# Kernel optimization log

Hardware: AMD Instinct MI355X
Metric: run time of the kernel (lower is better)

The kernel has to match this reference:

```python
import jax, jax.numpy as jnp
import numpy as np

B, C, H, W = 4, 96, 64, 64
N_STATE, DT_RANK, K = 16, 6, 3


def _layernorm(x, g, b, eps=1e-5):
    m = jnp.mean(x, axis=-1, keepdims=True)
    v = jnp.mean((x - m) ** 2, axis=-1, keepdims=True)
    return (x - m) / jnp.sqrt(v + eps) * g + b


def _grid_sample(img, gx, gy):
    # F.grid_sample: bilinear, align_corners=True, zeros padding; gx,gy in [-1,1], [B,Ho,Wo]
    Bc, Cc, Hi, Wi = img.shape
    fx = (gx + 1.0) * 0.5 * (Wi - 1)
    fy = (gy + 1.0) * 0.5 * (Hi - 1)
    x0 = jnp.floor(fx)
    y0 = jnp.floor(fy)
    wx1 = fx - x0
    wy1 = fy - y0

    def tap(ix, iy, w):
        valid = ((ix >= 0) & (ix < Wi) & (iy >= 0) & (iy < Hi)).astype(img.dtype)
        ic = jnp.clip(ix, 0, Wi - 1).astype(jnp.int32)
        jc = jnp.clip(iy, 0, Hi - 1).astype(jnp.int32)
        v = jax.vmap(lambda im, yy, xx: im[:, yy, xx])(img, jc, ic)  # [B,C,Ho,Wo]
        return v * (w * valid)[:, None, :, :]

    return (tap(x0, y0, (1 - wx1) * (1 - wy1)) + tap(x0 + 1, y0, wx1 * (1 - wy1))
            + tap(x0, y0 + 1, (1 - wx1) * wy1) + tap(x0 + 1, y0 + 1, wx1 * wy1))


def _resize_bilinear(img, Ho, Wo):
    # torch F.interpolate(mode='bilinear', align_corners=False)
    Bc, Cc, Hi, Wi = img.shape

    def src(n_out, n_in):
        s = jnp.maximum((jnp.arange(n_out, dtype=img.dtype) + 0.5) * (n_in / n_out) - 0.5, 0.0)
        i0 = jnp.floor(s).astype(jnp.int32)
        i1 = jnp.minimum(i0 + 1, n_in - 1)
        return i0, i1, s - i0

    y0, y1, wy = src(Ho, Hi)
    x0, x1, wx = src(Wo, Wi)
    row = img[:, :, y0, :] * (1 - wy)[None, None, :, None] + img[:, :, y1, :] * wy[None, None, :, None]
    return row[:, :, :, x0] * (1 - wx) + row[:, :, :, x1] * wx


def _conv_offset(x, conv1_w, conv1_b, ca1_w, ca1_b, ca2_w, ca2_b, ln_g, ln_b, conv2_w):
    Bc, Cc = x.shape[:2]
    p = conv1_w.shape[-1] // 2
    x1 = jax.lax.conv_general_dilated(
        x, conv1_w, (1, 1), [(p, p), (p, p)],
        dimension_numbers=("NCHW", "OIHW", "NCHW"), feature_group_count=Cc
    ) + conv1_b[None, :, None, None]
    xc = jnp.mean(x, axis=(2, 3))  # adaptive_avg_pool2d -> (1,1)
    hid = jax.nn.gelu(xc @ ca1_w.T + ca1_b, approximate=False)
    ca = jax.nn.sigmoid(hid @ ca2_w.T + ca2_b)
    x1 = x1 * ca[:, :, None, None]
    xn = _layernorm(jnp.transpose(x1, (0, 2, 3, 1)), ln_g, ln_b)
    xg = jax.nn.gelu(jnp.transpose(xn, (0, 3, 1, 2)), approximate=False)
    return jnp.einsum("bchw,oc->bohw", xg, conv2_w[:, :, 0, 0])


def _deformable(x, rpe_table, conv1_w, conv1_b, ca1_w, ca1_b, ca2_w, ca2_b, ln_g, ln_b, conv2_w):
    Bc, Cc, Hc, Wc = x.shape
    L = Hc * Wc
    off = _conv_offset(x, conv1_w, conv1_b, ca1_w, ca1_b, ca2_w, ca2_b, ln_g, ln_b, conv2_w)
    offset = off[:, :2]
    de = off[:, 2]
    rng = jnp.array([1.0 / (Hc - 1.0), 1.0 / (Wc - 1.0)], off.dtype).reshape(1, 2, 1, 1)
    offset = jnp.transpose(jnp.tanh(offset) * rng, (0, 2, 3, 1))  # [B,H,W,2] (dy,dx)
    ry = (jnp.linspace(0.5, Hc - 0.5, Hc) / (Hc - 1.0)) * 2.0 - 1.0
    rx = (jnp.linspace(0.5, Wc - 0.5, Wc) / (Wc - 1.0)) * 2.0 - 1.0
    ref = jnp.stack(jnp.meshgrid(ry, rx, indexing="ij"), -1)  # [H,W,2] (y,x)
    pos = offset + ref[None]
    de_index = jnp.tanh(de).reshape(Bc, L)
    path_ref = (jnp.linspace(0.5, L - 0.5, L) / (L - 1.0)) * 2.0 - 1.0
    path_pos = de_index + path_ref[None]
    x_sampled = _grid_sample(x, pos[..., 1], pos[..., 0])
    rpe = jnp.broadcast_to(rpe_table[None], (Bc,) + rpe_table.shape)
    rpe_bias = _resize_bilinear(rpe, Hc, Wc)
    ky = (jnp.linspace(0.0, float(Hc), Hc) / (Hc - 1.0)) * 2.0 - 1.0
    kx = (jnp.linspace(0.0, float(Wc), Wc) / (Wc - 1.0)) * 2.0 - 1.0
    key_grid = jnp.stack(jnp.meshgrid(ky, kx, indexing="ij"), -1)
    disp = (key_grid[None] - pos) * 0.5
    pos_bias = _grid_sample(rpe_bias, disp[..., 1], disp[..., 0])
    xd = (x_sampled + pos_bias).reshape(Bc, Cc, L)
    indices = jnp.argsort(path_pos, axis=-1)  # topk(k=N, largest=False) == ascending argsort
    xs2 = jnp.take_along_axis(xd, indices[:, None, :], axis=2)
    return xs2, indices


def _selective_scan(u, delta, A, Bs, Cs, Dv, delta_bias):
    Bc, KD, L = u.shape
    Kk = Bs.shape[1]
    Dd = KD // Kk
    Ns = A.shape[1]
    delta = jax.nn.softplus(delta + delta_bias[None, :, None])
    dt4 = jnp.moveaxis(delta.reshape(Bc, Kk, Dd, L), 3, 0)
    u4 = jnp.moveaxis(u.reshape(Bc, Kk, Dd, L), 3, 0)
    Bt = jnp.moveaxis(Bs, 3, 0)
    Ct = jnp.moveaxis(Cs, 3, 0)
    A3 = A.reshape(Kk, Dd, Ns)

    @jax.checkpoint
    def step(h, inp):
        dt, ut, bt, ct = inp  # [B,K,D],[B,K,D],[B,K,N],[B,K,N]
        h = jnp.exp(dt[..., None] * A3) * h + (dt * ut)[..., None] * bt[:, :, None, :]
        return h, jnp.einsum("bkdn,bkn->bkd", h, ct)

    h0 = jnp.zeros((Bc, Kk, Dd, Ns), u.dtype)
    _, ys = jax.lax.scan(step, h0, (dt4, u4, Bt, Ct))
    ys = jnp.moveaxis(ys, 0, 3).reshape(Bc, KD, L)
    return ys + u * Dv[None, :, None]


def _forward(x, x_proj_weight, dt_projs_weight, dt_projs_bias, A_logs, Ds_param,
             conv1_w, conv1_b, ca1_w, ca1_b, ca2_w, ca2_b, ln_g, ln_b, conv2_w, rpe_table):
    Bc, Dd, Hc, Wc = x.shape
    L = Hc * Wc
    Kk, _, R = dt_projs_weight.shape
    Ns = A_logs.shape[1]
    xs0 = x.reshape(Bc, Dd, L)
    xs2, indices = _deformable(x, rpe_table, conv1_w, conv1_b, ca1_w, ca1_b, ca2_w, ca2_b, ln_g, ln_b, conv2_w)
    xs = jnp.stack([xs0, xs0[..., ::-1], xs2], axis=1)  # [B,3,D,L]
    x_dbl = jnp.einsum("bkdl,kcd->bkcl", xs, x_proj_weight)
    dts, Bs, Cs = jnp.split(x_dbl, [R, R + Ns], axis=2)
    dts = jnp.einsum("bkrl,kdr->bkdl", dts, dt_projs_weight)
    A = -jnp.exp(A_logs)
    ys = _selective_scan(xs.reshape(Bc, Kk * Dd, L), dts.reshape(Bc, Kk * Dd, L),
                         A, Bs, Cs, Ds_param, dt_projs_bias.reshape(-1))
    ys = ys.reshape(Bc, Kk, Dd, L)
    inv = jnp.argsort(indices, axis=-1)  # inverse permutation (DeformableLayerReverse)
    y2 = jnp.take_along_axis(ys[:, 2], inv[:, None, :], axis=2)
    y = (ys[:, 0] + ys[:, 1][..., ::-1] + y2) / 3.0
    return jnp.transpose(y, (0, 2, 1)).reshape(Bc, Hc, Wc, Dd)


def setup_inputs():
    key = jax.random.key(0)
    ks = jax.random.split(key, 12)
    f = jnp.float32
    return {
        "x": jax.random.normal(ks[0], (B, C, H, W), f),
        "x_proj_weight": jax.random.normal(ks[1], (K, DT_RANK + 2 * N_STATE, C), f) * 0.05,
        "dt_projs_weight": jax.random.normal(ks[2], (K, C, DT_RANK), f) * 0.05,
        "dt_projs_bias": jax.random.normal(ks[3], (K, C), f) * 0.1,
        "A_logs": jnp.tile(jnp.log(jnp.arange(1, N_STATE + 1, dtype=f))[None, :], (K * C, 1)),
        "Ds_param": jnp.ones((K * C,), f),
        "conv1_w": jax.random.normal(ks[4], (C, 1, 9, 9), f) * 0.05,
        "conv1_b": jnp.zeros((C,), f),
        "ca1_w": jax.random.normal(ks[5], (C // 16, C), f) * 0.1,
        "ca1_b": jnp.zeros((C // 16,), f),
        "ca2_w": jax.random.normal(ks[6], (C, C // 16), f) * 0.1,
        "ca2_b": jnp.zeros((C,), f),
        "ln_g": jnp.ones((C,), f),
        "ln_b": jnp.zeros((C,), f),
        "conv2_w": jax.random.normal(ks[7], (3, C, 1, 1), f) * 0.05,
        "rpe_table": jax.random.normal(ks[8], (C, 7, 7), f) * 0.01,
    }


def reference(x, x_proj_weight, dt_projs_weight, dt_projs_bias, A_logs, Ds_param,
              conv1_w, conv1_b, ca1_w, ca1_b, ca2_w, ca2_b, ln_g, ln_b, conv2_w, rpe_table):
    return _forward(x, x_proj_weight, dt_projs_weight, dt_projs_bias, A_logs, Ds_param,
                    conv1_w, conv1_b, ca1_w, ca1_b, ca2_w, ca2_b, ln_g, ln_b, conv2_w, rpe_table)
```

## Files before the change

### kernel.cpp

```cpp
#include <hip/hip_runtime.h>

#define BB 4
#define CC 96
#define HH 64
#define WW 64
#define LL 4096
#define KK 3
#define RR 6
#define NN 16

__device__ __forceinline__ float geluf(float x){
    return 0.5f * x * (1.0f + erff(x * 0.70710678118654752f));
}
__device__ __forceinline__ float softplusf(float x){
    return fmaxf(x, 0.0f) + log1pf(expf(-fabsf(x)));
}
__device__ __forceinline__ float sigmoidf(float x){
    return 1.0f / (1.0f + expf(-x));
}

__global__ __launch_bounds__(256) void k_mean(const float* __restrict__ x, float* __restrict__ xc){
    int bc = blockIdx.x;
    const float* p = x + (size_t)bc * LL;
    float s = 0.f;
    for (int i = threadIdx.x; i < LL; i += 256) s += p[i];
    __shared__ float red[256];
    red[threadIdx.x] = s; __syncthreads();
    for (int st = 128; st > 0; st >>= 1){
        if (threadIdx.x < st) red[threadIdx.x] += red[threadIdx.x + st];
        __syncthreads();
    }
    if (threadIdx.x == 0) xc[bc] = red[0] * (1.0f / LL);
}

__global__ __launch_bounds__(128) void k_ca(const float* __restrict__ xc,
                     const float* __restrict__ w1, const float* __restrict__ b1,
                     const float* __restrict__ w2, const float* __restrict__ b2,
                     float* __restrict__ ca){
    int b = blockIdx.x;
    int t = threadIdx.x;
    __shared__ float hid[CC/16];
    if (t < CC/16){
        float a = b1[t];
        for (int d = 0; d < CC; d++) a += w1[t*CC + d] * xc[b*CC + d];
        hid[t] = geluf(a);
    }
    __syncthreads();
    if (t < CC){
        float a = b2[t];
        #pragma unroll
        for (int i = 0; i < CC/16; i++) a += w2[t*(CC/16) + i] * hid[i];
        ca[b*CC + t] = sigmoidf(a);
    }
}

__global__ __launch_bounds__(256) void k_conv(const float* __restrict__ x, const float* __restrict__ w,
                       const float* __restrict__ bias, const float* __restrict__ ca,
                       float* __restrict__ x1){
    int tid4 = blockIdx.x * 256 + threadIdx.x;
    int wq4 = (tid4 & 15) * 4;
    int rest = tid4 >> 4;
    int h = rest & 63;
    int bc = rest >> 6;
    int c = bc % CC; int b = bc / CC;
    const float* xp = x + (size_t)bc * LL;
    const float* wp = w + c * 81;
    float a0 = 0.f, a1 = 0.f, a2 = 0.f, a3 = 0.f;
    #pragma unroll
    for (int ky = 0; ky < 9; ky++){
        int yy = h + ky - 4;
        if (yy < 0 || yy >= HH) continue;
        const float4* row4 = (const float4*)(xp + yy*WW);
        int g = wq4 >> 2;
        float4 q0 = (wq4 >= 4)  ? row4[g-1] : make_float4(0.f,0.f,0.f,0.f);
        float4 q1 = row4[g];
        float4 q2 = (wq4 < 60)  ? row4[g+1] : make_float4(0.f,0.f,0.f,0.f);
        float v[12] = {q0.x,q0.y,q0.z,q0.w, q1.x,q1.y,q1.z,q1.w, q2.x,q2.y,q2.z,q2.w};
        const float* wr = wp + ky*9;
        #pragma unroll
        for (int kx = 0; kx < 9; kx++){
            float wk = wr[kx];
            a0 = fmaf(v[kx],   wk, a0);
            a1 = fmaf(v[kx+1], wk, a1);
            a2 = fmaf(v[kx+2], wk, a2);
            a3 = fmaf(v[kx+3], wk, a3);
        }
    }
    float sc = ca[b*CC + c];
    float bb = bias[c];
    float4 o = make_float4((a0+bb)*sc, (a1+bb)*sc, (a2+bb)*sc, (a3+bb)*sc);
    *(float4*)(x1 + (size_t)bc*LL + h*WW + wq4) = o;
}

__global__ __launch_bounds__(256) void k_rpe(const float* __restrict__ t, float* __restrict__ out){
    int gid = blockIdx.x * 256 + threadIdx.x;
    int l = gid & (LL-1); int c = gid >> 12;
    int h = l >> 6, w = l & 63;
    float sy = fmaxf((h + 0.5f) * (7.0f/64.0f) - 0.5f, 0.f);
    float sx = fmaxf((w + 0.5f) * (7.0f/64.0f) - 0.5f, 0.f);
    int y0 = (int)floorf(sy); int x0 = (int)floorf(sx);
    float wy = sy - (float)y0, wx = sx - (float)x0;
    int y1 = min(y0 + 1, 6), x1i = min(x0 + 1, 6);
    const float* tp = t + c * 49;
    float r0 = tp[y0*7 + x0] * (1.f - wy) + tp[y1*7 + x0] * wy;
    float r1 = tp[y0*7 + x1i] * (1.f - wy) + tp[y1*7 + x1i] * wy;
    out[gid] = r0 * (1.f - wx) + r1 * wx;
}

__global__ __launch_bounds__(256) void k_off(const float* __restrict__ x1,
                      const float* __restrict__ g, const float* __restrict__ bta,
                      const float* __restrict__ w2,
                      float* __restrict__ posy, float* __restrict__ posx, float* __restrict__ path){
    int blk = blockIdx.x;
    int ltile = blk & 63; int b = blk >> 6;
    int lane = threadIdx.x & 63;
    int wg = threadIdx.x >> 6;
    int l = ltile * 64 + lane;
    const float* p = x1 + (size_t)b * CC * LL + l;
    float v[24];
    float s = 0.f, ss = 0.f;
    #pragma unroll
    for (int j = 0; j < 24; j++){
        float t = p[(size_t)(wg*24 + j) * LL];
        v[j] = t; s += t; ss += t*t;
    }
    __shared__ float ls[4][64], lss[4][64];
    ls[wg][lane] = s; lss[wg][lane] = ss;
    __syncthreads();
    s  = ls[0][lane]  + ls[1][lane]  + ls[2][lane]  + ls[3][lane];
    ss = lss[0][lane] + lss[1][lane] + lss[2][lane] + lss[3][lane];
    float m = s * (1.0f/CC);
    float rstd = rsqrtf(ss*(1.0f/CC) - m*m + 1e-5f);
    float a0 = 0.f, a1 = 0.f, a2 = 0.f;
    #pragma unroll
    for (int j = 0; j < 24; j++){
        int c = wg*24 + j;
        float xn = (v[j]-m)*rstd*g[c] + bta[c];
        float xg = geluf(xn);
        a0 = fmaf(w2[c],      xg, a0);
        a1 = fmaf(w2[CC+c],   xg, a1);
        a2 = fmaf(w2[2*CC+c], xg, a2);
    }
    __shared__ float la[3][4][64];
    la[0][wg][lane] = a0; la[1][wg][lane] = a1; la[2][wg][lane] = a2;
    __syncthreads();
    if (wg < 3){
        float a = la[wg][0][lane] + la[wg][1][lane] + la[wg][2][lane] + la[wg][3][lane];
        int h = l >> 6, w = l & 63;
        if (wg == 0)      posy[b*LL + l] = tanhf(a)*(1.0f/63.0f) + ((2*h+1)*(1.0f/63.0f) - 1.0f);
        else if (wg == 1) posx[b*LL + l] = tanhf(a)*(1.0f/63.0f) + ((2*w+1)*(1.0f/63.0f) - 1.0f);
        else              path[b*LL + l] = tanhf(a) + ((l + 0.5f)*(2.0f/4095.0f) - 1.0f);
    }
}

__device__ __forceinline__ float bilin0(const float* __restrict__ img, float gx, float gy){
    float fx = (gx + 1.f) * 31.5f;
    float fy = (gy + 1.f) * 31.5f;
    float x0f = floorf(fx), y0f = floorf(fy);
    float wx = fx - x0f, wy = fy - y0f;
    int x0 = (int)x0f, y0 = (int)y0f;
    float acc = 0.f;
    bool vx0 = (x0 >= 0) & (x0 < WW), vx1 = (x0+1 >= 0) & (x0+1 < WW);
    bool vy0 = (y0 >= 0) & (y0 < HH), vy1 = (y0+1 >= 0) & (y0+1 < HH);
    if (vy0 & vx0) acc += img[y0*WW + x0]       * (1.f-wx) * (1.f-wy);
    if (vy0 & vx1) acc += img[y0*WW + x0+1]     * wx       * (1.f-wy);
    if (vy1 & vx0) acc += img[(y0+1)*WW + x0]   * (1.f-wx) * wy;
    if (vy1 & vx1) acc += img[(y0+1)*WW + x0+1] * wx       * wy;
    return acc;
}

typedef unsigned long long u64s;
__device__ __forceinline__ u64s shflx64(u64s x, int m){
    int lo = __shfl_xor((int)(unsigned)x, m);
    int hi = __shfl_xor((int)(unsigned)(x >> 32), m);
    return ((u64s)(unsigned)hi << 32) | (unsigned)lo;
}
__device__ __forceinline__ void cex(u64s& a, u64s& b, bool up){
    u64s mn = a < b ? a : b;
    u64s mx = a < b ? b : a;
    a = up ? mn : mx;
    b = up ? mx : mn;
}
__global__ __launch_bounds__(1024) void k_sortsample(
        const float* __restrict__ path, int* __restrict__ idx, int* __restrict__ inv,
        const float* __restrict__ x, const float* __restrict__ rpe,
        const float* __restrict__ posy, const float* __restrict__ posx,
        float* __restrict__ xd){
    int blk = blockIdx.x;
    if (blk < BB){
        int b = blk;
        int t = threadIdx.x;
        __shared__ u64s lds[LL];
        u64s v[4];
        #pragma unroll
        for (int r = 0; r < 4; r++){
            int e = t*4 + r;
            unsigned u = __float_as_uint(path[b*LL + e]);
            u ^= (u >> 31) ? 0xFFFFFFFFu : 0x80000000u;
            v[r] = ((u64s)u << 32) | (unsigned)e;
        }
        for (int kk = 2; kk <= LL; kk <<= 1){
            for (int j = kk >> 1; j > 0; j >>= 1){
                if (j >= 256){
                    __syncthreads();
                    #pragma unroll
                    for (int r = 0; r < 4; r++) lds[t*4 + r] = v[r];
                    __syncthreads();
                    #pragma unroll
                    for (int r = 0; r < 4; r++){
                        int e = t*4 + r;
                        u64s pv = lds[e ^ j];
                        bool up    = ((e & kk) == 0);
                        bool lower = ((e & j) == 0);
                        u64s mn = v[r] < pv ? v[r] : pv;
                        u64s mx = v[r] < pv ? pv : v[r];
                        v[r] = (up == lower) ? mn : mx;
                    }
                } else if (j >= 4){
                    int m = j >> 2;
                    #pragma unroll
                    for (int r = 0; r < 4; r++){
                        u64s pv = shflx64(v[r], m);
                        bool up    = (((t*4 + r) & kk) == 0);
                        bool lower = ((t & m) == 0);
                        u64s mn = v[r] < pv ? v[r] : pv;
                        u64s mx = v[r] < pv ? pv : v[r];
                        v[r] = (up == lower) ? mn : mx;
                    }
                } else if (j == 2){
                    bool up = (((t*4) & kk) == 0);
                    cex(v[0], v[2], up);
                    cex(v[1], v[3], up);
                } else {
                    if (kk == 2){
                        cex(v[0], v[1], true);
                        cex(v[2], v[3], false);
                    } else {
                        bool up = (((t*4) & kk) == 0);
                        cex(v[0], v[1], up);
                        cex(v[2], v[3], up);
                    }
                }
            }
        }
        #pragma unroll
        for (int r = 0; r < 4; r++){
            int e = t*4 + r;
            int id = (int)(unsigned)(v[r] & 0xFFFFFFFFu);
            idx[b*LL + e] = id;
            inv[b*LL + id] = e;
        }
    } else {
        int gid = (blk - BB) * 1024 + threadIdx.x;
        int l = gid & (LL-1); int bc = gid >> 12;
        int b = bc / CC; int c = bc % CC;
        float gy = posy[b*LL + l], gx = posx[b*LL + l];
        float v = bilin0(x + (size_t)bc * LL, gx, gy);
        int h = l >> 6, w = l & 63;
        float ky = h * (128.0f/3969.0f) - 1.0f;
        float kx = w * (128.0f/3969.0f) - 1.0f;
        float v2 = bilin0(rpe + (size_t)c * LL, (kx - gx) * 0.5f, (ky - gy) * 0.5f);
        xd[gid] = v + v2;
    }
}

__global__ __launch_bounds__(192, 1) void k_proj(const float* __restrict__ x, const float* __restrict__ xd,
    const int* __restrict__ indices, const float* __restrict__ xpw, const float* __restrict__ dtw,
    const float* __restrict__ dtb, float* __restrict__ u2, float* __restrict__ dt,
    float* __restrict__ Bst, float* __restrict__ Cst){
    int blk = blockIdx.x;
    int ltile = blk & 63; int bk = blk >> 6;
    int k = bk % KK; int b = bk / KK;
    int lane = threadIdx.x & 63;
    int w = threadIdx.x >> 6;
    const float* __restrict__ Wk = xpw + k*38*CC;
    int l = ltile * 64 + lane;
    int srcl = (k == 0) ? l : (k == 1 ? (LL-1-l) : indices[b*LL + l]);
    const float* xp = (k == 2 ? xd : x) + (size_t)b * CC * LL + srcl;

    __shared__ float vsh[CC*64];
    #pragma unroll
    for (int j = 0; j < 32; j++){
        int d = w*32 + j;
        vsh[d*64 + lane] = xp[(size_t)d * LL];
    }
    __syncthreads();

    if (w == 0){
        float acc[RR];
        #pragma unroll
        for (int i = 0; i < RR; i++) acc[i] = 0.f;
        for (int d = 0; d < CC; d++){
            float vv = vsh[d*64 + lane];
            #pragma unroll
            for (int i = 0; i < RR; i++) acc[i] = fmaf(Wk[i*CC + d], vv, acc[i]);
        }
        const float* __restrict__ Dw = dtw + k*CC*RR;
        const float* __restrict__ Db = dtb + k*CC;
        float* dtp = dt + (size_t)bk * CC * LL + l;
        #pragma unroll 8
        for (int d = 0; d < CC; d++){
            float sdt = Db[d];
            #pragma unroll
            for (int r = 0; r < RR; r++) sdt = fmaf(acc[r], Dw[d*RR + r], sdt);
            dtp[(size_t)d * LL] = softplusf(sdt);
        }
    } else if (w == 1){
        float acc[NN];
        #pragma unroll
        for (int i = 0; i < NN; i++) acc[i] = 0.f;
        for (int d = 0; d < CC; d++){
            float vv = vsh[d*64 + lane];
            #pragma unroll
            for (int i = 0; i < NN; i++) acc[i] = fmaf(Wk[(RR + i)*CC + d], vv, acc[i]);
        }
        size_t base = ((size_t)bk * LL + l) * NN;
        #pragma unroll
        for (int q = 0; q < 4; q++){
            float4 o; o.x = acc[q*4]; o.y = acc[q*4+1]; o.z = acc[q*4+2]; o.w = acc[q*4+3];
            *(float4*)(Bst + base + q*4) = o;
        }
    } else {
        float acc[NN];
        #pragma unroll
        for (int i = 0; i < NN; i++) acc[i] = 0.f;
        for (int d = 0; d < CC; d++){
            float vv = vsh[d*64 + lane];
            #pragma unroll
            for (int i = 0; i < NN; i++) acc[i] = fmaf(Wk[(RR + NN + i)*CC + d], vv, acc[i]);
        }
        size_t base = ((size_t)bk * LL + l) * NN;
        #pragma unroll
        for (int q = 0; q < 4; q++){
            float4 o; o.x = acc[q*4]; o.y = acc[q*4+1]; o.z = acc[q*4+2]; o.w = acc[q*4+3];
            *(float4*)(Cst + base + q*4) = o;
        }
        if (k == 2){
            float* up = u2 + (size_t)b * CC * LL + l;
            #pragma unroll 8
            for (int d = 0; d < CC; d++) up[(size_t)d * LL] = vsh[d*64 + lane];
        }
    }
}

#define SEG 128
#define TL 32
#define SROW 17
#define XROW 32
template<int KIND>
__device__ __forceinline__ void scan_body(int b, int d, const float* __restrict__ usrc,
    const float* __restrict__ dt, const float* __restrict__ Bst, const float* __restrict__ Cst,
    const float* __restrict__ Alog, const float* __restrict__ Ds, float* __restrict__ ys,
    float* sA, float* sB, float* sS, float* yl){
    int bk = b * KK + KIND;
    int tid = threadIdx.x;
    int ng = tid & 3;
    int seg = tid >> 2;
    int t0 = seg * TL;
    int xsw = (seg & 7) << 2;

    const float4 A4 = *(const float4*)(Alog + (KIND*CC + d)*NN + 4*ng);
    const float L2E = 1.4426950408889634f;
    float A2[4] = { -__expf(A4.x)*L2E, -__expf(A4.y)*L2E, -__expf(A4.z)*L2E, -__expf(A4.w)*L2E };
    float Dv = Ds[KIND*CC + d];

    const float* dtp = dt + ((size_t)bk * CC + d) * LL + t0;
    const float* ub = (KIND == 1)
        ? usrc + ((size_t)b*CC + d) * LL + (LL-4-t0)
        : usrc + ((size_t)b*CC + d) * LL + t0;
    const float* Bp = Bst + ((size_t)bk * LL + t0) * NN + 4*ng;
    const float* Cp = Cst + ((size_t)bk * LL + t0) * NN + 4*ng;
    float* yp = ys + ((size_t)bk * CC + d) * LL + t0;

    float h[4] = {0.f,0.f,0.f,0.f};
    float S = 0.f;
    for (int t = 0; t < TL; t += 4){
        float4 dq = *(const float4*)(dtp + t);
        float4 uq = (KIND == 1) ? *(const float4*)(ub - t) : *(const float4*)(ub + t);
        float4 Bq[4], Cq[4];
        #pragma unroll
        for (int i = 0; i < 4; i++){
            Bq[i] = *(const float4*)(Bp + (t+i)*NN);
            Cq[i] = *(const float4*)(Cp + (t+i)*NN);
        }
        float dd[4] = {dq.x, dq.y, dq.z, dq.w};
        float uu[4];
        if (KIND == 1){ uu[0]=uq.w; uu[1]=uq.z; uu[2]=uq.y; uu[3]=uq.x; }
        else          { uu[0]=uq.x; uu[1]=uq.y; uu[2]=uq.z; uu[3]=uq.w; }
        float sv[4], pv[4];
        #pragma unroll
        for (int i = 0; i < 4; i++){
            float du = dd[i] * uu[i];
            float bb[4] = {Bq[i].x, Bq[i].y, Bq[i].z, Bq[i].w};
            float cc[4] = {Cq[i].x, Cq[i].y, Cq[i].z, Cq[i].w};
            float p = 0.f;
            #pragma unroll
            for (int j = 0; j < 4; j++){
                float a = exp2f(dd[i] * A2[j]);
                h[j] = fmaf(a, h[j], du * bb[j]);
                p = fmaf(h[j], cc[j], p);
            }
            S += dd[i];
            sv[i] = S;
            p += __shfl_xor(p, 1);
            p += __shfl_xor(p, 2);
            pv[i] = fmaf(uu[i], Dv, p);
        }
        if (ng == 0){
            int xo = seg*XROW + (t ^ xsw);
            *(float4*)(sS + xo) = make_float4(sv[0], sv[1], sv[2], sv[3]);
            *(float4*)(yl + xo) = make_float4(pv[0], pv[1], pv[2], pv[3]);
        }
    }

    #pragma unroll
    for (int j = 0; j < 4; j++){
        sA[seg*SROW + 4*ng + j] = exp2f(A2[j] * S);
        sB[seg*SROW + 4*ng + j] = h[j];
    }
    __syncthreads();
    {
        int wv = tid >> 6;
        int lane = tid & 63;
        #pragma unroll
        for (int nn = 0; nn < 2; nn++){
            int n = 2*wv + nn;
            float a1 = sA[(2*lane)*SROW + n],   b1 = sB[(2*lane)*SROW + n];
            float a2 = sA[(2*lane+1)*SROW + n], b2 = sB[(2*lane+1)*SROW + n];
            float ca = a1 * a2;
            float cb = fmaf(a2, b1, b2);
            #pragma unroll
            for (int off = 1; off < 64; off <<= 1){
                float ta = __shfl_up(ca, off);
                float tb = __shfl_up(cb, off);
                if (lane >= off){
                    cb = fmaf(ca, tb, cb);
                    ca *= ta;
                }
            }
            float cb_prev = __shfl_up(cb, 1);
            if (lane == 0) cb_prev = 0.f;
            sA[(2*lane)*SROW + n]   = cb_prev;
            sA[(2*lane+1)*SROW + n] = fmaf(a1, cb_prev, b1);
        }
    }
    __syncthreads();
    float hc[4];
    #pragma unroll
    for (int j = 0; j < 4; j++) hc[j] = sA[seg*SROW + 4*ng + j];

    for (int t = 0; t < TL; t += 4){
        int xo = seg*XROW + (t ^ xsw);
        float4 sq = *(const float4*)(sS + xo);
        float4 Cq[4];
        #pragma unroll
        for (int i = 0; i < 4; i++) Cq[i] = *(const float4*)(Cp + (t+i)*NN);
        float sv[4] = {sq.x, sq.y, sq.z, sq.w};
        float yo[4];
        #pragma unroll
        for (int i = 0; i < 4; i++){
            float cc[4] = {Cq[i].x, Cq[i].y, Cq[i].z, Cq[i].w};
            float corr = 0.f;
            #pragma unroll
            for (int j = 0; j < 4; j++){
                float P = exp2f(sv[i] * A2[j]);
                corr = fmaf(P * hc[j], cc[j], corr);
            }
            corr += __shfl_xor(corr, 1);
            corr += __shfl_xor(corr, 2);
            yo[i] = corr;
        }
        if (ng == 0){
            float4 ylq = *(const float4*)(yl + xo);
            float4 o = make_float4(ylq.x + yo[0], ylq.y + yo[1], ylq.z + yo[2], ylq.w + yo[3]);
            *(float4*)(yp + t) = o;
        }
    }
}

__global__ __launch_bounds__(512) void k_scan_all(const float* __restrict__ x, const float* __restrict__ u2,
    const float* __restrict__ dt, const float* __restrict__ Bst, const float* __restrict__ Cst,
    const float* __restrict__ Alog, const float* __restrict__ Ds, float* __restrict__ ys){
    __shared__ float sA[SEG*SROW];
    __shared__ float sB[SEG*SROW];
    __shared__ float sS[SEG*XROW];
    __shared__ float yl[SEG*XROW];
    int blk = blockIdx.x;
    int k = blk / (BB*CC);
    int r = blk % (BB*CC);
    int d = r % CC; int b = r / CC;
    if (k == 0)      scan_body<0>(b, d, x,  dt, Bst, Cst, Alog, Ds, ys, sA, sB, sS, yl);
    else if (k == 1) scan_body<1>(b, d, x,  dt, Bst, Cst, Alog, Ds, ys, sA, sB, sS, yl);
    else             scan_body<2>(b, d, u2, dt, Bst, Cst, Alog, Ds, ys, sA, sB, sS, yl);
}

__global__ __launch_bounds__(256) void k_comb(const float* __restrict__ ys, const int* __restrict__ inv,
                                              float* __restrict__ out){
    int tile = blockIdx.x & 255; int b = blockIdx.x >> 8;
    int l0 = tile * 16;
    __shared__ float t0[CC * 17];
    __shared__ int invs[16];
    if (threadIdx.x < 16) invs[threadIdx.x] = inv[b*LL + l0 + threadIdx.x];
    __syncthreads();
    const float* y0p = ys + (size_t)(b*KK + 0) * CC * LL;
    const float* y1p = ys + (size_t)(b*KK + 1) * CC * LL;
    const float* y2p = ys + (size_t)(b*KK + 2) * CC * LL;
    #pragma unroll
    for (int it = 0; it < 6; it++){
        int e = it * 256 + threadIdx.x;
        int li = e & 15; int c = e >> 4;
        int l = l0 + li;
        float v = y0p[(size_t)c*LL + l] + y1p[(size_t)c*LL + (LL-1-l)] + y2p[(size_t)c*LL + invs[li]];
        t0[c*17 + li] = v * (1.0f/3.0f);
    }
    __syncthreads();
    #pragma unroll
    for (int it = 0; it < 6; it++){
        int e = it * 256 + threadIdx.x;
        int c = e % CC; int li = e / CC;
        out[((size_t)b*LL + l0 + li) * CC + c] = t0[c*17 + li];
    }
}

extern "C" void kernel_launch(void* const* d_in, const int* in_sizes, int n_in,
                              void* d_out, int out_size, void* d_ws, size_t ws_size,
                              hipStream_t stream){
    const float* x    = (const float*)d_in[0];
    const float* xpw  = (const float*)d_in[1];
    const float* dtw  = (const float*)d_in[2];
    const float* dtb  = (const float*)d_in[3];
    const float* Alog = (const float*)d_in[4];
    const float* Ds   = (const float*)d_in[5];
    const float* c1w  = (const float*)d_in[6];
    const float* c1b  = (const float*)d_in[7];
    const float* ca1w = (const float*)d_in[8];
    const float* ca1b = (const float*)d_in[9];
    const float* ca2w = (const float*)d_in[10];
    const float* ca2b = (const float*)d_in[11];
    const float* lng  = (const float*)d_in[12];
    const float* lnb  = (const float*)d_in[13];
    const float* c2w  = (const float*)d_in[14];
    const float* rpet = (const float*)d_in[15];
    float* out = (float*)d_out;

    float* ws   = (float*)d_ws;
    float* xc   = ws;
    float* ca   = xc + 384;
    float* x1   = ca + 384;
    float* rpe  = x1 + (size_t)BB*CC*LL;
    float* posy = rpe + (size_t)CC*LL;
    float* posx = posy + (size_t)BB*LL;
    float* path = posx + (size_t)BB*LL;
    float* xd   = path + (size_t)BB*LL;
    int*   idx  = (int*)(xd + (size_t)BB*CC*LL);
    int*   inv  = idx + (size_t)BB*LL;
    float* u2   = (float*)(inv + (size_t)BB*LL);
    float* dtA  = u2 + (size_t)BB*CC*LL;
    float* Bst  = dtA + (size_t)BB*KK*CC*LL;
    float* Cst  = Bst + (size_t)BB*KK*LL*NN;
    float* ysA  = Cst + (size_t)BB*KK*LL*NN;

    k_mean  <<<BB*CC, 256, 0, stream>>>(x, xc);
    k_ca    <<<BB, 128, 0, stream>>>(xc, ca1w, ca1b, ca2w, ca2b, ca);
    k_conv  <<<(BB*CC*LL/4)/256, 256, 0, stream>>>(x, c1w, c1b, ca, x1);
    k_rpe   <<<(CC*LL)/256, 256, 0, stream>>>(rpet, rpe);
    k_off   <<<BB*64, 256, 0, stream>>>(x1, lng, lnb, c2w, posy, posx, path);
    k_sortsample<<<BB + (BB*CC*LL)/1024, 1024, 0, stream>>>(path, idx, inv, x, rpe, posy, posx, xd);
    k_proj  <<<BB*KK*64, 192, 0, stream>>>(x, xd, idx, xpw, dtw, dtb, u2, dtA, Bst, Cst);
    k_scan_all<<<KK*BB*CC, 512, 0, stream>>>(x, u2, dtA, Bst, Cst, Alog, Ds, ysA);
    k_comb  <<<BB*256, 256, 0, stream>>>(ysA, inv, out);
}
```

Baseline: 295.8 us.

## Co-schedule independent stages in shared launches to overlap projection, scan and combine

Reorders the pipeline so that independent work shares kernel launches. The channel mean is merged with the RPE resize. The k=0/1 projections run alongside the depthwise conv. The k=2 projection runs alongside the k=0/1 scans. The k=2 scan runs alongside a partial combine of directions 0 and 1, and a final kernel adds the gathered direction 2. The goal is to fill idle CUs and cut the serial dependency chain and launch count. The offset kernel is also retiled to 32 positions by 8 channel groups. The trade-offs are mixed block shapes inside one launch, a read-modify-write of the output, and load imbalance between heterogeneous block types.

```diff
diff --git a/kernel.cpp b/kernel.cpp
--- a/kernel.cpp
+++ b/kernel.cpp
@@ -19,18 +19,34 @@
     return 1.0f / (1.0f + expf(-x));
 }
 
-__global__ __launch_bounds__(256) void k_mean(const float* __restrict__ x, float* __restrict__ xc){
-    int bc = blockIdx.x;
-    const float* p = x + (size_t)bc * LL;
-    float s = 0.f;
-    for (int i = threadIdx.x; i < LL; i += 256) s += p[i];
-    __shared__ float red[256];
-    red[threadIdx.x] = s; __syncthreads();
-    for (int st = 128; st > 0; st >>= 1){
-        if (threadIdx.x < st) red[threadIdx.x] += red[threadIdx.x + st];
-        __syncthreads();
-    }
-    if (threadIdx.x == 0) xc[bc] = red[0] * (1.0f / LL);
+__global__ __launch_bounds__(256) void k_meanrpe(const float* __restrict__ x, float* __restrict__ xc,
+                                                 const float* __restrict__ rpet, float* __restrict__ rpe){
+    int blk = blockIdx.x;
+    if (blk < BB*CC){
+        const float* p = x + (size_t)blk * LL;
+        float s = 0.f;
+        for (int i = threadIdx.x; i < LL; i += 256) s += p[i];
+        __shared__ float red[256];
+        red[threadIdx.x] = s; __syncthreads();
+        for (int st = 128; st > 0; st >>= 1){
+            if (threadIdx.x < st) red[threadIdx.x] += red[threadIdx.x + st];
+            __syncthreads();
+        }
+        if (threadIdx.x == 0) xc[blk] = red[0] * (1.0f / LL);
+    } else {
+        int gid = (blk - BB*CC) * 256 + threadIdx.x;
+        int l = gid & (LL-1); int c = gid >> 12;
+        int h = l >> 6, w = l & 63;
+        float sy = fmaxf((h + 0.5f) * (7.0f/64.0f) - 0.5f, 0.f);
+        float sx = fmaxf((w + 0.5f) * (7.0f/64.0f) - 0.5f, 0.f);
+        int y0 = (int)floorf(sy); int x0 = (int)floorf(sx);
+        float wy = sy - (float)y0, wx = sx - (float)x0;
+        int y1 = min(y0 + 1, 6), x1i = min(x0 + 1, 6);
+        const float* tp = rpet + c * 49;
+        float r0 = tp[y0*7 + x0] * (1.f - wy) + tp[y1*7 + x0] * wy;
+        float r1 = tp[y0*7 + x1i] * (1.f - wy) + tp[y1*7 + x1i] * wy;
+        rpe[gid] = r0 * (1.f - wx) + r1 * wx;
+    }
 }
 
 __global__ __launch_bounds__(128) void k_ca(const float* __restrict__ xc,
@@ -54,57 +70,134 @@
     }
 }
 
-__global__ __launch_bounds__(256) void k_conv(const float* __restrict__ x, const float* __restrict__ w,
+__device__ __forceinline__ void proj_sub(int b, int k, int ltile, int sub_tid,
+    const float* __restrict__ x, const float* __restrict__ xd, const int* __restrict__ indices,
+    const float* __restrict__ xpw, const float* __restrict__ dtw, const float* __restrict__ dtb,
+    float* __restrict__ u2, float* __restrict__ dt,
+    float* __restrict__ Bst, float* __restrict__ Cst, float* vsh){
+    int lane = sub_tid & 63;
+    int w = sub_tid >> 6;
+    int bk = b * KK + k;
+    const float* __restrict__ Wk = xpw + k*38*CC;
+    int l = ltile * 64 + lane;
+    int srcl = (k == 0) ? l : (k == 1 ? (LL-1-l) : indices[b*LL + l]);
+    const float* xp = (k == 2 ? xd : x) + (size_t)b * CC * LL + srcl;
+
+    #pragma unroll
+    for (int j = 0; j < 24; j++){
+        int d = w*24 + j;
+        vsh[d*64 + lane] = xp[(size_t)d * LL];
+    }
+    __syncthreads();
+
+    if (w == 0 || w == 3){
+        float acc[RR];
+        #pragma unroll
+        for (int i = 0; i < RR; i++) acc[i] = 0.f;
+        for (int d = 0; d < CC; d++){
+            float vv = vsh[d*64 + lane];
+            #pragma unroll
+            for (int i = 0; i < RR; i++) acc[i] = fmaf(Wk[i*CC + d], vv, acc[i]);
+        }
+        const float* __restrict__ Dw = dtw + k*CC*RR;
+        const float* __restrict__ Db = dtb + k*CC;
+        float* dtp = dt + (size_t)bk * CC * LL + l;
+        int dlo = (w == 0) ? 0 : 48;
+        #pragma unroll 8
+        for (int d = dlo; d < dlo + 48; d++){
+            float sdt = Db[d];
+            #pragma unroll
+            for (int r = 0; r < RR; r++) sdt = fmaf(acc[r], Dw[d*RR + r], sdt);
+            dtp[(size_t)d * LL] = softplusf(sdt);
+        }
+    } else if (w == 1){
+        float acc[NN];
+        #pragma unroll
+        for (int i = 0; i < NN; i++) acc[i] = 0.f;
+        for (int d = 0; d < CC; d++){
+            float vv = vsh[d*64 + lane];
+            #pragma unroll
+            for (int i = 0; i < NN; i++) acc[i] = fmaf(Wk[(RR + i)*CC + d], vv, acc[i]);
+        }
+        size_t base = ((size_t)bk * LL + l) * NN;
+        #pragma unroll
+        for (int q = 0; q < 4; q++){
+            float4 o; o.x = acc[q*4]; o.y = acc[q*4+1]; o.z = acc[q*4+2]; o.w = acc[q*4+3];
+            *(float4*)(Bst + base + q*4) = o;
+        }
+    } else {
+        float acc[NN];
+        #pragma unroll
+        for (int i = 0; i < NN; i++) acc[i] = 0.f;
+        for (int d = 0; d < CC; d++){
+            float vv = vsh[d*64 + lane];
+            #pragma unroll
+            for (int i = 0; i < NN; i++) acc[i] = fmaf(Wk[(RR + NN + i)*CC + d], vv, acc[i]);
+        }
+        size_t base = ((size_t)bk * LL + l) * NN;
+        #pragma unroll
+        for (int q = 0; q < 4; q++){
+            float4 o; o.x = acc[q*4]; o.y = acc[q*4+1]; o.z = acc[q*4+2]; o.w = acc[q*4+3];
+            *(float4*)(Cst + base + q*4) = o;
+        }
+        if (k == 2){
+            float* up = u2 + (size_t)b * CC * LL + l;
+            #pragma unroll 8
+            for (int d = 0; d < CC; d++) up[(size_t)d * LL] = vsh[d*64 + lane];
+        }
+    }
+}
+
+__global__ __launch_bounds__(256) void k_convproj(const float* __restrict__ x, const float* __restrict__ w,
                        const float* __restrict__ bias, const float* __restrict__ ca,
-                       float* __restrict__ x1){
-    int tid4 = blockIdx.x * 256 + threadIdx.x;
-    int wq4 = (tid4 & 15) * 4;
-    int rest = tid4 >> 4;
-    int h = rest & 63;
-    int bc = rest >> 6;
-    int c = bc % CC; int b = bc / CC;
-    const float* xp = x + (size_t)bc * LL;
-    const float* wp = w + c * 81;
-    float a0 = 0.f, a1 = 0.f, a2 = 0.f, a3 = 0.f;
-    #pragma unroll
-    for (int ky = 0; ky < 9; ky++){
-        int yy = h + ky - 4;
-        if (yy < 0 || yy >= HH) continue;
-        const float4* row4 = (const float4*)(xp + yy*WW);
-        int g = wq4 >> 2;
-        float4 q0 = (wq4 >= 4)  ? row4[g-1] : make_float4(0.f,0.f,0.f,0.f);
-        float4 q1 = row4[g];
-        float4 q2 = (wq4 < 60)  ? row4[g+1] : make_float4(0.f,0.f,0.f,0.f);
-        float v[12] = {q0.x,q0.y,q0.z,q0.w, q1.x,q1.y,q1.z,q1.w, q2.x,q2.y,q2.z,q2.w};
-        const float* wr = wp + ky*9;
-        #pragma unroll
-        for (int kx = 0; kx < 9; kx++){
-            float wk = wr[kx];
-            a0 = fmaf(v[kx],   wk, a0);
-            a1 = fmaf(v[kx+1], wk, a1);
-            a2 = fmaf(v[kx+2], wk, a2);
-            a3 = fmaf(v[kx+3], wk, a3);
-        }
-    }
-    float sc = ca[b*CC + c];
-    float bb = bias[c];
-    float4 o = make_float4((a0+bb)*sc, (a1+bb)*sc, (a2+bb)*sc, (a3+bb)*sc);
-    *(float4*)(x1 + (size_t)bc*LL + h*WW + wq4) = o;
-}
-
-__global__ __launch_bounds__(256) void k_rpe(const float* __restrict__ t, float* __restrict__ out){
-    int gid = blockIdx.x * 256 + threadIdx.x;
-    int l = gid & (LL-1); int c = gid >> 12;
-    int h = l >> 6, w = l & 63;
-    float sy = fmaxf((h + 0.5f) * (7.0f/64.0f) - 0.5f, 0.f);
-    float sx = fmaxf((w + 0.5f) * (7.0f/64.0f) - 0.5f, 0.f);
-    int y0 = (int)floorf(sy); int x0 = (int)floorf(sx);
-    float wy = sy - (float)y0, wx = sx - (float)x0;
-    int y1 = min(y0 + 1, 6), x1i = min(x0 + 1, 6);
-    const float* tp = t + c * 49;
-    float r0 = tp[y0*7 + x0] * (1.f - wy) + tp[y1*7 + x0] * wy;
-    float r1 = tp[y0*7 + x1i] * (1.f - wy) + tp[y1*7 + x1i] * wy;
-    out[gid] = r0 * (1.f - wx) + r1 * wx;
+                       float* __restrict__ x1,
+                       const float* __restrict__ xpw, const float* __restrict__ dtw,
+                       const float* __restrict__ dtb, float* __restrict__ dt,
+                       float* __restrict__ Bst, float* __restrict__ Cst){
+    __shared__ float vsh[CC*64];
+    int blk = blockIdx.x;
+    if (blk < (BB*CC*LL/4)/256){
+        int tid4 = blk * 256 + threadIdx.x;
+        int wq4 = (tid4 & 15) * 4;
+        int rest = tid4 >> 4;
+        int h = rest & 63;
+        int bc = rest >> 6;
+        int c = bc % CC; int b = bc / CC;
+        const float* xp = x + (size_t)bc * LL;
+        const float* wp = w + c * 81;
+        float a0 = 0.f, a1 = 0.f, a2 = 0.f, a3 = 0.f;
+        #pragma unroll
+        for (int ky = 0; ky < 9; ky++){
+            int yy = h + ky - 4;
+            if (yy < 0 || yy >= HH) continue;
+            const float4* row4 = (const float4*)(xp + yy*WW);
+            int g = wq4 >> 2;
+            float4 q0 = (wq4 >= 4)  ? row4[g-1] : make_float4(0.f,0.f,0.f,0.f);
+            float4 q1 = row4[g];
+            float4 q2 = (wq4 < 60)  ? row4[g+1] : make_float4(0.f,0.f,0.f,0.f);
+            float v[12] = {q0.x,q0.y,q0.z,q0.w, q1.x,q1.y,q1.z,q1.w, q2.x,q2.y,q2.z,q2.w};
+            const float* wr = wp + ky*9;
+            #pragma unroll
+            for (int kx = 0; kx < 9; kx++){
+                float wk = wr[kx];
+                a0 = fmaf(v[kx],   wk, a0);
+                a1 = fmaf(v[kx+1], wk, a1);
+                a2 = fmaf(v[kx+2], wk, a2);
+                a3 = fmaf(v[kx+3], wk, a3);
+            }
+        }
+        float sc = ca[b*CC + c];
+        float bb = bias[c];
+        float4 o = make_float4((a0+bb)*sc, (a1+bb)*sc, (a2+bb)*sc, (a3+bb)*sc);
+        *(float4*)(x1 + (size_t)bc*LL + h*WW + wq4) = o;
+    } else {
+        int pj = blk - (BB*CC*LL/4)/256;
+        int ltile = pj & 63;
+        int bkq = pj >> 6;
+        int b = bkq >> 1; int k = bkq & 1;
+        proj_sub(b, k, ltile, threadIdx.x, x, (const float*)0, (const int*)0,
+                 xpw, dtw, dtb, (float*)0, dt, Bst, Cst, vsh);
+    }
 }
 
 __global__ __launch_bounds__(256) void k_off(const float* __restrict__ x1,
@@ -112,43 +205,46 @@
                       const float* __restrict__ w2,
                       float* __restrict__ posy, float* __restrict__ posx, float* __restrict__ path){
     int blk = blockIdx.x;
-    int ltile = blk & 63; int b = blk >> 6;
-    int lane = threadIdx.x & 63;
-    int wg = threadIdx.x >> 6;
-    int l = ltile * 64 + lane;
+    int tile = blk & 127; int b = blk >> 7;
+    int li = threadIdx.x & 31;
+    int cg = threadIdx.x >> 5;
+    int l = tile * 32 + li;
     const float* p = x1 + (size_t)b * CC * LL + l;
-    float v[24];
+    float v[12];
     float s = 0.f, ss = 0.f;
     #pragma unroll
-    for (int j = 0; j < 24; j++){
-        float t = p[(size_t)(wg*24 + j) * LL];
+    for (int j = 0; j < 12; j++){
+        float t = p[(size_t)(cg*12 + j) * LL];
         v[j] = t; s += t; ss += t*t;
     }
-    __shared__ float ls[4][64], lss[4][64];
-    ls[wg][lane] = s; lss[wg][lane] = ss;
-    __syncthreads();
-    s  = ls[0][lane]  + ls[1][lane]  + ls[2][lane]  + ls[3][lane];
-    ss = lss[0][lane] + lss[1][lane] + lss[2][lane] + lss[3][lane];
+    __shared__ float ls[8][32], lss[8][32];
+    ls[cg][li] = s; lss[cg][li] = ss;
+    __syncthreads();
+    s = 0.f; ss = 0.f;
+    #pragma unroll
+    for (int g2 = 0; g2 < 8; g2++){ s += ls[g2][li]; ss += lss[g2][li]; }
     float m = s * (1.0f/CC);
     float rstd = rsqrtf(ss*(1.0f/CC) - m*m + 1e-5f);
     float a0 = 0.f, a1 = 0.f, a2 = 0.f;
     #pragma unroll
-    for (int j = 0; j < 24; j++){
-        int c = wg*24 + j;
+    for (int j = 0; j < 12; j++){
+        int c = cg*12 + j;
         float xn = (v[j]-m)*rstd*g[c] + bta[c];
         float xg = geluf(xn);
         a0 = fmaf(w2[c],      xg, a0);
         a1 = fmaf(w2[CC+c],   xg, a1);
         a2 = fmaf(w2[2*CC+c], xg, a2);
     }
-    __shared__ float la[3][4][64];
-    la[0][wg][lane] = a0; la[1][wg][lane] = a1; la[2][wg][lane] = a2;
-    __syncthreads();
-    if (wg < 3){
-        float a = la[wg][0][lane] + la[wg][1][lane] + la[wg][2][lane] + la[wg][3][lane];
-        int h = l >> 6, w = l & 63;
-        if (wg == 0)      posy[b*LL + l] = tanhf(a)*(1.0f/63.0f) + ((2*h+1)*(1.0f/63.0f) - 1.0f);
-        else if (wg == 1) posx[b*LL + l] = tanhf(a)*(1.0f/63.0f) + ((2*w+1)*(1.0f/63.0f) - 1.0f);
+    __shared__ float la[3][8][32];
+    la[0][cg][li] = a0; la[1][cg][li] = a1; la[2][cg][li] = a2;
+    __syncthreads();
+    if (cg < 3){
+        float a = 0.f;
+        #pragma unroll
+        for (int g2 = 0; g2 < 8; g2++) a += la[cg][g2][li];
+        int h = l >> 6, ww = l & 63;
+        if (cg == 0)      posy[b*LL + l] = tanhf(a)*(1.0f/63.0f) + ((2*h+1)*(1.0f/63.0f) - 1.0f);
+        else if (cg == 1) posx[b*LL + l] = tanhf(a)*(1.0f/63.0f) + ((2*ww+1)*(1.0f/63.0f) - 1.0f);
         else              path[b*LL + l] = tanhf(a) + ((l + 0.5f)*(2.0f/4095.0f) - 1.0f);
     }
 }
@@ -264,85 +360,6 @@
     }
 }
 
-__global__ __launch_bounds__(192, 1) void k_proj(const float* __restrict__ x, const float* __restrict__ xd,
-    const int* __restrict__ indices, const float* __restrict__ xpw, const float* __restrict__ dtw,
-    const float* __restrict__ dtb, float* __restrict__ u2, float* __restrict__ dt,
-    float* __restrict__ Bst, float* __restrict__ Cst){
-    int blk = blockIdx.x;
-    int ltile = blk & 63; int bk = blk >> 6;
-    int k = bk % KK; int b = bk / KK;
-    int lane = threadIdx.x & 63;
-    int w = threadIdx.x >> 6;
-    const float* __restrict__ Wk = xpw + k*38*CC;
-    int l = ltile * 64 + lane;
-    int srcl = (k == 0) ? l : (k == 1 ? (LL-1-l) : indices[b*LL + l]);
-    const float* xp = (k == 2 ? xd : x) + (size_t)b * CC * LL + srcl;
-
-    __shared__ float vsh[CC*64];
-    #pragma unroll
-    for (int j = 0; j < 32; j++){
-        int d = w*32 + j;
-        vsh[d*64 + lane] = xp[(size_t)d * LL];
-    }
-    __syncthreads();
-
-    if (w == 0){
-        float acc[RR];
-        #pragma unroll
-        for (int i = 0; i < RR; i++) acc[i] = 0.f;
-        for (int d = 0; d < CC; d++){
-            float vv = vsh[d*64 + lane];
-            #pragma unroll
-            for (int i = 0; i < RR; i++) acc[i] = fmaf(Wk[i*CC + d], vv, acc[i]);
-        }
-        const float* __restrict__ Dw = dtw + k*CC*RR;
-        const float* __restrict__ Db = dtb + k*CC;
-        float* dtp = dt + (size_t)bk * CC * LL + l;
-        #pragma unroll 8
-        for (int d = 0; d < CC; d++){
-            float sdt = Db[d];
-            #pragma unroll
-            for (int r = 0; r < RR; r++) sdt = fmaf(acc[r], Dw[d*RR + r], sdt);
-            dtp[(size_t)d * LL] = softplusf(sdt);
-        }
-    } else if (w == 1){
-        float acc[NN];
-        #pragma unroll
-        for (int i = 0; i < NN; i++) acc[i] = 0.f;
-        for (int d = 0; d < CC; d++){
-            float vv = vsh[d*64 + lane];
-            #pragma unroll
-            for (int i = 0; i < NN; i++) acc[i] = fmaf(Wk[(RR + i)*CC + d], vv, acc[i]);
-        }
-        size_t base = ((size_t)bk * LL + l) * NN;
-        #pragma unroll
-        for (int q = 0; q < 4; q++){
-            float4 o; o.x = acc[q*4]; o.y = acc[q*4+1]; o.z = acc[q*4+2]; o.w = acc[q*4+3];
-            *(float4*)(Bst + base + q*4) = o;
-        }
-    } else {
-        float acc[NN];
-        #pragma unroll
-        for (int i = 0; i < NN; i++) acc[i] = 0.f;
-        for (int d = 0; d < CC; d++){
-            float vv = vsh[d*64 + lane];
-            #pragma unroll
-            for (int i = 0; i < NN; i++) acc[i] = fmaf(Wk[(RR + NN + i)*CC + d], vv, acc[i]);
-        }
-        size_t base = ((size_t)bk * LL + l) * NN;
-        #pragma unroll
-        for (int q = 0; q < 4; q++){
-            float4 o; o.x = acc[q*4]; o.y = acc[q*4+1]; o.z = acc[q*4+2]; o.w = acc[q*4+3];
-            *(float4*)(Cst + base + q*4) = o;
-        }
-        if (k == 2){
-            float* up = u2 + (size_t)b * CC * LL + l;
-            #pragma unroll 8
-            for (int d = 0; d < CC; d++) up[(size_t)d * LL] = vsh[d*64 + lane];
-        }
-    }
-}
-
 #define SEG 128
 #define TL 32
 #define SROW 17
@@ -478,47 +495,93 @@
     }
 }
 
-__global__ __launch_bounds__(512) void k_scan_all(const float* __restrict__ x, const float* __restrict__ u2,
+__global__ __launch_bounds__(512) void k_projscan(const float* __restrict__ x, const float* __restrict__ xd,
+    const int* __restrict__ indices, const float* __restrict__ xpw, const float* __restrict__ dtw,
+    const float* __restrict__ dtb, float* __restrict__ u2, float* __restrict__ dt,
+    float* __restrict__ Bst, float* __restrict__ Cst,
+    const float* __restrict__ Alog, const float* __restrict__ Ds, float* __restrict__ ys){
+    __shared__ float smem[12544];
+    int blk = blockIdx.x;
+    if (blk < 128){
+        int s = threadIdx.x >> 8;
+        int sub_tid = threadIdx.x & 255;
+        int pj = blk*2 + s;
+        int ltile = pj & 63; int b = pj >> 6;
+        proj_sub(b, 2, ltile, sub_tid, x, xd, indices, xpw, dtw, dtb,
+                 u2, dt, Bst, Cst, smem + s*6144);
+    } else {
+        int sblk = blk - 128;
+        int k = sblk / (BB*CC);
+        int r = sblk % (BB*CC);
+        int d = r % CC; int b = r / CC;
+        float* sA = smem;
+        float* sB = smem + SEG*SROW;
+        float* sS = smem + 2*SEG*SROW;
+        float* yl = smem + 2*SEG*SROW + SEG*XROW;
+        if (k == 0) scan_body<0>(b, d, x, dt, Bst, Cst, Alog, Ds, ys, sA, sB, sS, yl);
+        else        scan_body<1>(b, d, x, dt, Bst, Cst, Alog, Ds, ys, sA, sB, sS, yl);
+    }
+}
+
+__global__ __launch_bounds__(512) void k_scan2comb(const float* __restrict__ u2,
     const float* __restrict__ dt, const float* __restrict__ Bst, const float* __restrict__ Cst,
-    const float* __restrict__ Alog, const float* __restrict__ Ds, float* __restrict__ ys){
-    __shared__ float sA[SEG*SROW];
-    __shared__ float sB[SEG*SROW];
-    __shared__ float sS[SEG*XROW];
-    __shared__ float yl[SEG*XROW];
+    const float* __restrict__ Alog, const float* __restrict__ Ds, float* __restrict__ ys,
+    float* __restrict__ out){
+    __shared__ float smem[12544];
     int blk = blockIdx.x;
-    int k = blk / (BB*CC);
-    int r = blk % (BB*CC);
-    int d = r % CC; int b = r / CC;
-    if (k == 0)      scan_body<0>(b, d, x,  dt, Bst, Cst, Alog, Ds, ys, sA, sB, sS, yl);
-    else if (k == 1) scan_body<1>(b, d, x,  dt, Bst, Cst, Alog, Ds, ys, sA, sB, sS, yl);
-    else             scan_body<2>(b, d, u2, dt, Bst, Cst, Alog, Ds, ys, sA, sB, sS, yl);
-}
-
-__global__ __launch_bounds__(256) void k_comb(const float* __restrict__ ys, const int* __restrict__ inv,
-                                              float* __restrict__ out){
+    if (blk < BB*CC){
+        int d = blk % CC; int b = blk / CC;
+        float* sA = smem;
+        float* sB = smem + SEG*SROW;
+        float* sS = smem + 2*SEG*SROW;
+        float* yl = smem + 2*SEG*SROW + SEG*XROW;
+        scan_body<2>(b, d, u2, dt, Bst, Cst, Alog, Ds, ys, sA, sB, sS, yl);
+    } else {
+        int cb = blk - BB*CC;
+        int tile = cb & 127; int b = cb >> 7;
+        int l0 = tile * 32;
+        float* t0 = smem;
+        const float* y0p = ys + (size_t)(b*KK + 0) * CC * LL;
+        const float* y1p = ys + (size_t)(b*KK + 1) * CC * LL;
+        #pragma unroll
+        for (int it = 0; it < 6; it++){
+            int e = it * 512 + threadIdx.x;
+            int li = e & 31; int c = e >> 5;
+            int l = l0 + li;
+            float v = y0p[(size_t)c*LL + l] + y1p[(size_t)c*LL + (LL-1-l)];
+            t0[c*33 + li] = v * (1.0f/3.0f);
+        }
+        __syncthreads();
+        #pragma unroll
+        for (int it = 0; it < 6; it++){
+            int e = it * 512 + threadIdx.x;
+            int c = e % CC; int li = e / CC;
+            out[((size_t)b*LL + l0 + li) * CC + c] = t0[c*33 + li];
+        }
+    }
+}
+
+__global__ __launch_bounds__(256) void k_comb2(const float* __restrict__ ys, const int* __restrict__ inv,
+                                               float* __restrict__ out){
     int tile = blockIdx.x & 255; int b = blockIdx.x >> 8;
     int l0 = tile * 16;
     __shared__ float t0[CC * 17];
     __shared__ int invs[16];
     if (threadIdx.x < 16) invs[threadIdx.x] = inv[b*LL + l0 + threadIdx.x];
     __syncthreads();
-    const float* y0p = ys + (size_t)(b*KK + 0) * CC * LL;
-    const float* y1p = ys + (size_t)(b*KK + 1) * CC * LL;
     const float* y2p = ys + (size_t)(b*KK + 2) * CC * LL;
     #pragma unroll
     for (int it = 0; it < 6; it++){
         int e = it * 256 + threadIdx.x;
         int li = e & 15; int c = e >> 4;
-        int l = l0 + li;
-        float v = y0p[(size_t)c*LL + l] + y1p[(size_t)c*LL + (LL-1-l)] + y2p[(size_t)c*LL + invs[li]];
-        t0[c*17 + li] = v * (1.0f/3.0f);
+        t0[c*17 + li] = y2p[(size_t)c*LL + invs[li]] * (1.0f/3.0f);
     }
     __syncthreads();
     #pragma unroll
     for (int it = 0; it < 6; it++){
         int e = it * 256 + threadIdx.x;
         int c = e % CC; int li = e / CC;
-        out[((size_t)b*LL + l0 + li) * CC + c] = t0[c*17 + li];
+        out[((size_t)b*LL + l0 + li) * CC + c] += t0[c*17 + li];
     }
 }
 
@@ -560,13 +623,14 @@
     float* Cst  = Bst + (size_t)BB*KK*LL*NN;
     float* ysA  = Cst + (size_t)BB*KK*LL*NN;
 
-    k_mean  <<<BB*CC, 256, 0, stream>>>(x, xc);
-    k_ca    <<<BB, 128, 0, stream>>>(xc, ca1w, ca1b, ca2w, ca2b, ca);
-    k_conv  <<<(BB*CC*LL/4)/256, 256, 0, stream>>>(x, c1w, c1b, ca, x1);
-    k_rpe   <<<(CC*LL)/256, 256, 0, stream>>>(rpet, rpe);
-    k_off   <<<BB*64, 256, 0, stream>>>(x1, lng, lnb, c2w, posy, posx, path);
+    k_meanrpe  <<<BB*CC + (CC*LL)/256, 256, 0, stream>>>(x, xc, rpet, rpe);
+    k_ca       <<<BB, 128, 0, stream>>>(xc, ca1w, ca1b, ca2w, ca2b, ca);
+    k_convproj <<<(BB*CC*LL/4)/256 + 512, 256, 0, stream>>>(x, c1w, c1b, ca, x1,
+                                                            xpw, dtw, dtb, dtA, Bst, Cst);
+    k_off      <<<BB*128, 256, 0, stream>>>(x1, lng, lnb, c2w, posy, posx, path);
     k_sortsample<<<BB + (BB*CC*LL)/1024, 1024, 0, stream>>>(path, idx, inv, x, rpe, posy, posx, xd);
-    k_proj  <<<BB*KK*64, 192, 0, stream>>>(x, xd, idx, xpw, dtw, dtb, u2, dtA, Bst, Cst);
-    k_scan_all<<<KK*BB*CC, 512, 0, stream>>>(x, u2, dtA, Bst, Cst, Alog, Ds, ysA);
-    k_comb  <<<BB*256, 256, 0, stream>>>(ysA, inv, out);
-}
+    k_projscan <<<128 + 2*BB*CC, 512, 0, stream>>>(x, xd, idx, xpw, dtw, dtb, u2, dtA,
+                                                   Bst, Cst, Alog, Ds, ysA);
+    k_scan2comb<<<BB*CC + BB*128, 512, 0, stream>>>(u2, dtA, Bst, Cst, Alog, Ds, ysA, out);
+    k_comb2    <<<BB*256, 256, 0, stream>>>(ysA, inv, out);
+}
```

Result: no change. 296.4 us (+0.2%).
